# Kernel optimization log

Hardware: AMD Instinct MI355X
Metric: run time of the kernel (lower is better)

The kernel has to match this reference:

```python
import jax
import jax.numpy as jnp
import numpy as np
from jax import lax

B, L, A, C = 32, 128, 64, 128  # batch, length, n_agents, channels (in == out)
KT = 3                          # temporal kernel size, padding (KT-1)//2 keeps length


def setup_inputs() -> dict:
    key = jax.random.key(0)
    k1, k2, k3 = jax.random.split(key, 3)
    x = jax.random.normal(k1, (B, L, A, C), dtype=jnp.float32)
    # Conv2d weight [out_ch, in_ch, kt, 1] and bias, kaiming-ish scale
    W = jax.random.normal(k2, (C, C, KT, 1), dtype=jnp.float32) * (1.0 / np.sqrt(C * KT))
    b = jax.random.normal(k3, (C,), dtype=jnp.float32) * 0.01
    return {"x": x, "W": W, "b": b}


def reference(x, W, b):
    # x: [B, L, A, C] -> [B, C, L, A] (torch NCHW layout with H=time, W=agents)
    length, n_agents = x.shape[1], x.shape[2]
    xc = jnp.transpose(x, (0, 3, 1, 2))
    res = xc  # residual is identity (input_dim == output_dim, t_stride == 1)
    pad_t = (KT - 1) // 2
    y = lax.conv_general_dilated(
        xc, W,
        window_strides=(1, 1),
        padding=[(pad_t, pad_t), (0, 0)],
        dimension_numbers=("NCHW", "OIHW", "NCHW"),
    ) + b[None, :, None, None]  # [B, C, L, A]
    # Dense graph g[t,a,t',a'] = 1 iff t==t' or a==a'.  einsum('ncv,vw->ncw', x, g)
    # is exactly: sum over same time (all agents) + sum over same agent (all times) - self.
    agent_sum = jnp.sum(y, axis=3, keepdims=True)  # [B, C, L, 1]
    time_sum = jnp.sum(y, axis=2, keepdims=True)   # [B, C, 1, A]
    scale = (length + n_agents - 2) ** 0.5
    g = (agent_sum + time_sum - y) / scale
    out = jax.nn.relu(g + res)
    return jnp.transpose(out, (0, 2, 3, 1))  # [B, L, A, C]
```

## Files before the change

### kernel.cpp

```cpp
#include <hip/hip_runtime.h>
#include <stdint.h>


typedef __attribute__((ext_vector_type(8))) short bf16x8;
typedef __attribute__((ext_vector_type(4))) float f32x4;

__device__ __forceinline__ uint32_t f2bf(float f) {
    union { float f; uint32_t u; } v; v.f = f;
    return (v.u + 0x7FFFu + ((v.u >> 16) & 1u)) >> 16;
}
__device__ __forceinline__ float bf2f(uint32_t h) {
    union { uint32_t u; float f; } v; v.u = h << 16; return v.f;
}
__device__ __forceinline__ uint32_t pk2(float lo, float hi) {
    return f2bf(lo) | (f2bf(hi) << 16);
}

__global__ __launch_bounds__(256) void red_kernel(
    const float* __restrict__ x, uint16_t* __restrict__ xa16, float* __restrict__ xt_part,
    const float* __restrict__ W, uint16_t* __restrict__ wp)
{
    const int tid = threadIdx.x;
    const int bid = blockIdx.x;
    if (bid >= 512) {
        int o = (bid - 512) * 256 + tid;
        int i = o & 7, lane = (o >> 3) & 63, nt = (o >> 9) & 7, ks = (o >> 12) & 3, d = o >> 14;
        int ci = ks * 32 + (lane >> 4) * 8 + i;
        int co = nt * 16 + (lane & 15);
        wp[o] = (uint16_t)f2bf(W[(co * 128 + ci) * 3 + d]);
        return;
    }
    const int b = bid >> 4, g = bid & 15;
    const int ci8 = (tid & 15) * 8, ag = tid >> 4;
    __shared__ float red[16][128];

    float xtl[4][8];
    #pragma unroll
    for (int r = 0; r < 4; ++r)
        #pragma unroll
        for (int j = 0; j < 8; ++j) xtl[r][j] = 0.f;

    #pragma unroll
    for (int ti = 0; ti < 8; ++ti) {
        const int t = g * 8 + ti;
        const float* xr = x + ((size_t)(b * 128 + t) * 64) * 128;
        float s[8];
        #pragma unroll
        for (int j = 0; j < 8; ++j) s[j] = 0.f;
        #pragma unroll
        for (int r = 0; r < 4; ++r) {
            const int a = ag * 4 + r;
            const float4 v0 = *(const float4*)(xr + a * 128 + ci8);
            const float4 v1 = *(const float4*)(xr + a * 128 + ci8 + 4);
            s[0] += v0.x; s[1] += v0.y; s[2] += v0.z; s[3] += v0.w;
            s[4] += v1.x; s[5] += v1.y; s[6] += v1.z; s[7] += v1.w;
            xtl[r][0] += v0.x; xtl[r][1] += v0.y; xtl[r][2] += v0.z; xtl[r][3] += v0.w;
            xtl[r][4] += v1.x; xtl[r][5] += v1.y; xtl[r][6] += v1.z; xtl[r][7] += v1.w;
        }
        *(float4*)&red[ag][ci8]     = make_float4(s[0], s[1], s[2], s[3]);
        *(float4*)&red[ag][ci8 + 4] = make_float4(s[4], s[5], s[6], s[7]);
        __syncthreads();
        if (tid < 128) {
            float v = 0.f;
            #pragma unroll
            for (int i = 0; i < 16; ++i) v += red[i][tid];
            xa16[(size_t)(b * 130 + t + 1) * 128 + tid] = (uint16_t)f2bf(v);
        }
        __syncthreads();
    }
    if (g == 0 && tid < 16)
        *(uint4*)(xa16 + (size_t)(b * 130) * 128 + tid * 8) = make_uint4(0, 0, 0, 0);
    if (g == 15 && tid < 16)
        *(uint4*)(xa16 + (size_t)(b * 130 + 129) * 128 + tid * 8) = make_uint4(0, 0, 0, 0);
    #pragma unroll
    for (int r = 0; r < 4; ++r) {
        float* p = xt_part + (((size_t)(b * 16 + g) * 64 + ag * 4 + r) * 128) + ci8;
        *(float4*)p       = make_float4(xtl[r][0], xtl[r][1], xtl[r][2], xtl[r][3]);
        *(float4*)(p + 4) = make_float4(xtl[r][4], xtl[r][5], xtl[r][6], xtl[r][7]);
    }
}

__global__ __launch_bounds__(256) void xtr_kernel(
    const float* __restrict__ xt_part, float* __restrict__ xt)
{
    const int idx = blockIdx.x * 256 + threadIdx.x;
    const int row = idx >> 4, ci8 = (idx & 15) * 8;
    const int b = row >> 6, a = row & 63;
    float s[8];
    #pragma unroll
    for (int j = 0; j < 8; ++j) s[j] = 0.f;
    #pragma unroll
    for (int g2 = 0; g2 < 16; ++g2) {
        const float* p = xt_part + (((size_t)(b * 16 + g2) * 64 + a) * 128) + ci8;
        const float4 v0 = *(const float4*)p;
        const float4 v1 = *(const float4*)(p + 4);
        s[0] += v0.x; s[1] += v0.y; s[2] += v0.z; s[3] += v0.w;
        s[4] += v1.x; s[5] += v1.y; s[6] += v1.z; s[7] += v1.w;
    }
    float* q = xt + (size_t)row * 128 + ci8;
    *(float4*)q       = make_float4(s[0], s[1], s[2], s[3]);
    *(float4*)(q + 4) = make_float4(s[4], s[5], s[6], s[7]);
}

__global__ __launch_bounds__(256, 2) void sums_kernel(
    const uint16_t* __restrict__ xa16, const float* __restrict__ xt,
    const float* __restrict__ x, const uint16_t* __restrict__ wp,
    const float* __restrict__ bias, float* __restrict__ asum, float* __restrict__ tsum)
{
    __shared__ __align__(16) uint16_t slab[130 * 128];
    const int tid = threadIdx.x;
    const int lane = tid & 63, wid = tid >> 6;
    const int wm = wid >> 1, wn = wid & 1;
    const int lr = lane & 15, lg = lane >> 4;
    f32x4 acc[4][4];
    #pragma unroll
    for (int mi = 0; mi < 4; ++mi)
        #pragma unroll
        for (int ni = 0; ni < 4; ++ni) acc[mi][ni] = (f32x4)0.f;

    if (blockIdx.x < 32) {
        const int b = blockIdx.x;
        #pragma unroll
        for (int it = 0; it < 9; ++it) {
            const int gg = it * 256 + tid;
            if (gg < 2080) {
                const int row = gg >> 4, sp = gg & 15;
                const int sl = sp ^ (row & 7);
                *(uint4*)(slab + gg * 8) =
                    *(const uint4*)(xa16 + (size_t)(b * 130 + row) * 128 + sl * 8);
            }
        }
        __syncthreads();
        #pragma unroll
        for (int g = 0; g < 4; ++g)
            #pragma unroll
            for (int d = 0; d < 3; ++d) {
                bf16x8 bq[4], af[4];
                #pragma unroll
                for (int ni = 0; ni < 4; ++ni)
                    bq[ni] = *(const bf16x8*)(wp + (size_t)((((d * 4 + g) * 8) + wn * 4 + ni) * 64 + lane) * 8);
                #pragma unroll
                for (int mi = 0; mi < 4; ++mi) {
                    const int row = wm * 64 + mi * 16 + lr + d;
                    af[mi] = *(const bf16x8*)(slab + row * 128 + ((g * 4 + lg) ^ (row & 7)) * 8);
                }
                #pragma unroll
                for (int mi = 0; mi < 4; ++mi)
                    #pragma unroll
                    for (int ni = 0; ni < 4; ++ni)
                        acc[mi][ni] = __builtin_amdgcn_mfma_f32_16x16x32_bf16(af[mi], bq[ni], acc[mi][ni], 0, 0, 0);
            }
        #pragma unroll
        for (int ni = 0; ni < 4; ++ni) {
            const int col = wn * 64 + ni * 16 + lr;
            const float bv = 64.f * bias[col];
            #pragma unroll
            for (int mi = 0; mi < 4; ++mi)
                #pragma unroll
                for (int j = 0; j < 4; ++j) {
                    const int t = wm * 64 + mi * 16 + lg * 4 + j;
                    asum[((size_t)b * 128 + t) * 128 + col] = acc[mi][ni][j] + bv;
                }
        }
        return;
    }

    const int bid = blockIdx.x - 32;
    const int r = tid >> 1, h = tid & 1;
    const int grow = bid * 128 + r, sb = grow >> 6, sa = grow & 63;
    #pragma unroll
    for (int d = 0; d < 3; ++d) {
        {
            const float* Sp = xt + (size_t)grow * 128 + h * 64;
            const float* Ep = x + ((size_t)((sb * 128 + (d == 0 ? 127 : 0)) * 64 + sa)) * 128 + h * 64;
            #pragma unroll
            for (int k = 0; k < 8; ++k) {
                float4 f0 = *(const float4*)(Sp + k * 8);
                float4 f1 = *(const float4*)(Sp + k * 8 + 4);
                if (d != 1) {
                    const float4 e0 = *(const float4*)(Ep + k * 8);
                    const float4 e1 = *(const float4*)(Ep + k * 8 + 4);
                    f0.x -= e0.x; f0.y -= e0.y; f0.z -= e0.z; f0.w -= e0.w;
                    f1.x -= e1.x; f1.y -= e1.y; f1.z -= e1.z; f1.w -= e1.w;
                }
                uint4 o;
                o.x = pk2(f0.x, f0.y); o.y = pk2(f0.z, f0.w);
                o.z = pk2(f1.x, f1.y); o.w = pk2(f1.z, f1.w);
                const int sl = h * 8 + k;
                *(uint4*)(slab + r * 128 + (sl ^ (r & 7)) * 8) = o;
            }
        }
        __syncthreads();
        #pragma unroll
        for (int g = 0; g < 4; ++g) {
            bf16x8 bq[4], af[4];
            #pragma unroll
            for (int ni = 0; ni < 4; ++ni)
                bq[ni] = *(const bf16x8*)(wp + (size_t)((((d * 4 + g) * 8) + wn * 4 + ni) * 64 + lane) * 8);
            #pragma unroll
            for (int mi = 0; mi < 4; ++mi) {
                const int row = wm * 64 + mi * 16 + lr;
                af[mi] = *(const bf16x8*)(slab + row * 128 + ((g * 4 + lg) ^ (row & 7)) * 8);
            }
            #pragma unroll
            for (int mi = 0; mi < 4; ++mi)
                #pragma unroll
                for (int ni = 0; ni < 4; ++ni)
                    acc[mi][ni] = __builtin_amdgcn_mfma_f32_16x16x32_bf16(af[mi], bq[ni], acc[mi][ni], 0, 0, 0);
        }
        __syncthreads();
    }
    #pragma unroll
    for (int ni = 0; ni < 4; ++ni) {
        const int col = wn * 64 + ni * 16 + lr;
        const float bv = 128.f * bias[col];
        #pragma unroll
        for (int mi = 0; mi < 4; ++mi)
            #pragma unroll
            for (int j = 0; j < 4; ++j) {
                const int rg = bid * 128 + wm * 64 + mi * 16 + lg * 4 + j;
                tsum[(size_t)rg * 128 + col] = acc[mi][ni][j] + bv;
            }
    }
}

__global__ __launch_bounds__(512, 6) void conv_kernel(
    const float* __restrict__ x, const uint16_t* __restrict__ wp,
    const float* __restrict__ bias, const float* __restrict__ asum,
    const float* __restrict__ tsum, float* __restrict__ out)
{
    __shared__ __align__(16) uint16_t slab[2][192 * 64];
    const int tid = threadIdx.x;
    const int raw = blockIdx.x;
    const int bid = (raw & 7) * 512 + (raw >> 3);
    const int b = bid >> 7, t = bid & 127;
    const int lane = tid & 63, wid = tid >> 6;
    const int lr = lane & 15, lg = lane >> 4;

    f32x4 acc[4];
    #pragma unroll
    for (int mi = 0; mi < 4; ++mi) acc[mi] = (f32x4)0.f;

#define STAGE(c) do {                                                          \
    _Pragma("unroll")                                                          \
    for (int k = 0; k < 3; ++k) {                                              \
        const int ro  = lane >> 3;                                             \
        const int row = wid * 24 + k * 8 + ro;                                 \
        const int gl  = (lane & 7) ^ ro;                                       \
        const int tloc = t + (row >> 6) - 1;                                   \
        uint4 o4 = make_uint4(0, 0, 0, 0);                                     \
        if ((unsigned)tloc < 128u) {                                           \
            const float* s_ = x +                                              \
                ((size_t)((b * 128 + tloc) * 64 + (row & 63))) * 128 +         \
                (c) * 64 + gl * 8;                                             \
            const float4 v0 = *(const float4*)s_;                              \
            const float4 v1 = *(const float4*)(s_ + 4);                        \
            o4.x = pk2(v0.x, v0.y); o4.y = pk2(v0.z, v0.w);                    \
            o4.z = pk2(v1.x, v1.y); o4.w = pk2(v1.z, v1.w);                    \
        }                                                                      \
        *(uint4*)(&slab[c][wid * 1536 + k * 512 + lane * 8]) = o4;             \
    } } while (0)

#define MFMA_CHUNK(c) do {                                                     \
    _Pragma("unroll")                                                          \
    for (int d = 0; d < 3; ++d)                                                \
        _Pragma("unroll")                                                      \
        for (int g2 = 0; g2 < 2; ++g2) {                                       \
            const int ks = (c) * 2 + g2;                                       \
            bf16x8 bq, af[4];                                                  \
            bq = *(const bf16x8*)(wp +                                         \
                (size_t)((((d * 4 + ks) * 8) + wid) * 64 + lane) * 8);         \
            _Pragma("unroll")                                                  \
            for (int mi = 0; mi < 4; ++mi) {                                   \
                const int row = d * 64 + mi * 16 + lr;                         \
                af[mi] = *(const bf16x8*)(&slab[c][row * 64 +                  \
                    (((g2 * 4 + lg) ^ (row & 7)) * 8)]);                       \
            }                                                                  \
            _Pragma("unroll")                                                  \
            for (int mi = 0; mi < 4; ++mi)                                     \
                acc[mi] = __builtin_amdgcn_mfma_f32_16x16x32_bf16(             \
                    af[mi], bq, acc[mi], 0, 0, 0);                             \
        } } while (0)

    STAGE(0);
    __syncthreads();
    STAGE(1);
    MFMA_CHUNK(0);
    __syncthreads();
    MFMA_CHUNK(1);
    __syncthreads();

#undef STAGE
#undef MFMA_CHUNK

    {
        const int col = wid * 16 + lr;
        const float bv = bias[col];
        const int cbuf = col >> 6, cl = col & 63;
        #pragma unroll
        for (int mi = 0; mi < 4; ++mi)
            #pragma unroll
            for (int j = 0; j < 4; ++j) {
                const int a = mi * 16 + lg * 4 + j;
                slab[cbuf][a * 64 + (cl ^ ((a & 7) << 3))] = (uint16_t)f2bf(acc[mi][j] + bv);
            }
    }
    __syncthreads();

    {
        const float inv = 0.07254762501100116f;
        const int cg = tid & 15, rb = tid >> 4;
        const int cbuf = cg >> 3, cl8 = (cg & 7) * 8;
        const float* ap = asum + ((size_t)(b * 128 + t)) * 128 + cg * 8;
        const float4 as0 = *(const float4*)ap, as1 = *(const float4*)(ap + 4);
        const float av[8] = {as0.x, as0.y, as0.z, as0.w, as1.x, as1.y, as1.z, as1.w};
        #pragma unroll
        for (int j = 0; j < 2; ++j) {
            const int a = j * 32 + rb;
            const int swz = cl8 ^ ((a & 7) << 3);
            const uint4 yv = *(const uint4*)(&slab[cbuf][a * 64 + swz]);
            const uint4 xv = *(const uint4*)(&slab[cbuf][(64 + a) * 64 + swz]);
            const float* tp = tsum + ((size_t)(b * 64 + a)) * 128 + cg * 8;
            const float4 ts0 = *(const float4*)tp, ts1 = *(const float4*)(tp + 4);
            float yy[8], xx[8];
            yy[0] = bf2f(yv.x & 0xFFFFu); yy[1] = bf2f(yv.x >> 16);
            yy[2] = bf2f(yv.y & 0xFFFFu); yy[3] = bf2f(yv.y >> 16);
            yy[4] = bf2f(yv.z & 0xFFFFu); yy[5] = bf2f(yv.z >> 16);
            yy[6] = bf2f(yv.w & 0xFFFFu); yy[7] = bf2f(yv.w >> 16);
            xx[0] = bf2f(xv.x & 0xFFFFu); xx[1] = bf2f(xv.x >> 16);
            xx[2] = bf2f(xv.y & 0xFFFFu); xx[3] = bf2f(xv.y >> 16);
            xx[4] = bf2f(xv.z & 0xFFFFu); xx[5] = bf2f(xv.z >> 16);
            xx[6] = bf2f(xv.w & 0xFFFFu); xx[7] = bf2f(xv.w >> 16);
            const float tv[8] = {ts0.x, ts0.y, ts0.z, ts0.w, ts1.x, ts1.y, ts1.z, ts1.w};
            float o[8];
            #pragma unroll
            for (int i = 0; i < 8; ++i) {
                const float gg = (av[i] + tv[i] - yy[i]) * inv + xx[i];
                o[i] = gg > 0.f ? gg : 0.f;
            }
            float* op = out + ((size_t)((b * 128 + t) * 64 + a)) * 128 + cg * 8;
            *(float4*)op       = make_float4(o[0], o[1], o[2], o[3]);
            *(float4*)(op + 4) = make_float4(o[4], o[5], o[6], o[7]);
        }
    }
}

extern "C" void kernel_launch(void* const* d_in, const int* in_sizes, int n_in,
                              void* d_out, int out_size, void* d_ws, size_t ws_size,
                              hipStream_t stream) {
    const float* x    = (const float*)d_in[0];
    const float* W    = (const float*)d_in[1];
    const float* bias = (const float*)d_in[2];
    float* out = (float*)d_out;

    char* ws = (char*)d_ws;
    uint16_t* wp    = (uint16_t*)(ws);
    uint16_t* xa16  = (uint16_t*)(ws + 98304);
    float* xt_part  = (float*)(ws + 98304 + 1064960);
    float* xt       = (float*)(ws + 98304 + 1064960 + 16777216);
    float* asum     = (float*)(ws + 98304 + 1064960 + 16777216 + 1048576);
    float* tsum     = (float*)(ws + 98304 + 1064960 + 16777216 + 1048576 + 2097152);

    red_kernel  <<<704,  256, 0, stream>>>(x, xa16, xt_part, W, wp);
    xtr_kernel  <<<128,  256, 0, stream>>>(xt_part, xt);
    sums_kernel <<<48,   256, 0, stream>>>(xa16, xt, x, wp, bias, asum, tsum);
    conv_kernel <<<4096, 512, 0, stream>>>(x, wp, bias, asum, tsum, out);
}
```

Baseline: 114.9 us.

## Process eight timesteps per conv block with a rolling LDS ring of input slices

The conv kernel now handles 8 consecutive time steps per block instead of one, keeping a 4-slot LDS ring of bf16 input slices. Each x slice is loaded once and reused across the three temporal taps, where before each block re-read three slices. The next slice is prefetched into registers while MFMAs run on the current ones, and the tsum values are loaded once per block. The grid drops from 4096 to 512 blocks, which lowers parallelism and adds two barriers per step.

```diff
diff --git a/kernel.cpp b/kernel.cpp
--- a/kernel.cpp
+++ b/kernel.cpp
@@ -224,125 +224,143 @@
     }
 }
 
-__global__ __launch_bounds__(512, 6) void conv_kernel(
+__global__ __launch_bounds__(512, 4) void conv_kernel(
     const float* __restrict__ x, const uint16_t* __restrict__ wp,
     const float* __restrict__ bias, const float* __restrict__ asum,
     const float* __restrict__ tsum, float* __restrict__ out)
 {
-    __shared__ __align__(16) uint16_t slab[2][192 * 64];
+    __shared__ __align__(16) uint16_t ring[4][8192];
+    __shared__ __align__(16) uint16_t yb[8192];
+
     const int tid = threadIdx.x;
-    const int raw = blockIdx.x;
-    const int bid = (raw & 7) * 512 + (raw >> 3);
-    const int b = bid >> 7, t = bid & 127;
+    const int bid = blockIdx.x;
+    const int b = bid >> 4, t0 = (bid & 15) * 8;
     const int lane = tid & 63, wid = tid >> 6;
     const int lr = lane & 15, lg = lane >> 4;
 
-    f32x4 acc[4];
-    #pragma unroll
-    for (int mi = 0; mi < 4; ++mi) acc[mi] = (f32x4)0.f;
-
-#define STAGE(c) do {                                                          \
-    _Pragma("unroll")                                                          \
-    for (int k = 0; k < 3; ++k) {                                              \
-        const int ro  = lane >> 3;                                             \
-        const int row = wid * 24 + k * 8 + ro;                                 \
-        const int gl  = (lane & 7) ^ ro;                                       \
-        const int tloc = t + (row >> 6) - 1;                                   \
-        uint4 o4 = make_uint4(0, 0, 0, 0);                                     \
-        if ((unsigned)tloc < 128u) {                                           \
-            const float* s_ = x +                                              \
-                ((size_t)((b * 128 + tloc) * 64 + (row & 63))) * 128 +         \
-                (c) * 64 + gl * 8;                                             \
-            const float4 v0 = *(const float4*)s_;                              \
-            const float4 v1 = *(const float4*)(s_ + 4);                        \
-            o4.x = pk2(v0.x, v0.y); o4.y = pk2(v0.z, v0.w);                    \
-            o4.z = pk2(v1.x, v1.y); o4.w = pk2(v1.z, v1.w);                    \
-        }                                                                      \
-        *(uint4*)(&slab[c][wid * 1536 + k * 512 + lane * 8]) = o4;             \
+    const int srow = tid >> 3, pair = tid & 7, r7 = srow & 7;
+    const int sgbase = ((2 * pair) ^ r7) & ~1;
+    const bool sswap = (r7 & 1);
+    const float* xsrc0 = x + ((size_t)(b * 128) * 64 + srow) * 128 + sgbase * 8;
+    const int sdst = tid * 16;
+
+#define STAGE_LOAD(tau, h) do {                                                \
+    if ((unsigned)(tau) < 128u) {                                              \
+        const float* s_ = xsrc0 + (size_t)(tau) * 8192;                        \
+        h[0] = *(const float4*)s_;       h[1] = *(const float4*)(s_ + 4);      \
+        h[2] = *(const float4*)(s_ + 8); h[3] = *(const float4*)(s_ + 12);     \
+    } else {                                                                   \
+        h[0] = h[1] = h[2] = h[3] = make_float4(0.f, 0.f, 0.f, 0.f);           \
     } } while (0)
 
-#define MFMA_CHUNK(c) do {                                                     \
-    _Pragma("unroll")                                                          \
-    for (int d = 0; d < 3; ++d)                                                \
-        _Pragma("unroll")                                                      \
-        for (int g2 = 0; g2 < 2; ++g2) {                                       \
-            const int ks = (c) * 2 + g2;                                       \
-            bf16x8 bq, af[4];                                                  \
-            bq = *(const bf16x8*)(wp +                                         \
-                (size_t)((((d * 4 + ks) * 8) + wid) * 64 + lane) * 8);         \
-            _Pragma("unroll")                                                  \
-            for (int mi = 0; mi < 4; ++mi) {                                   \
-                const int row = d * 64 + mi * 16 + lr;                         \
-                af[mi] = *(const bf16x8*)(&slab[c][row * 64 +                  \
-                    (((g2 * 4 + lg) ^ (row & 7)) * 8)]);                       \
-            }                                                                  \
-            _Pragma("unroll")                                                  \
-            for (int mi = 0; mi < 4; ++mi)                                     \
-                acc[mi] = __builtin_amdgcn_mfma_f32_16x16x32_bf16(             \
-                    af[mi], bq, acc[mi], 0, 0, 0);                             \
-        } } while (0)
-
-    STAGE(0);
+#define STAGE_WRITE(slot, h) do {                                              \
+    uint4 lo_, hi_;                                                            \
+    lo_.x = pk2(h[0].x, h[0].y); lo_.y = pk2(h[0].z, h[0].w);                  \
+    lo_.z = pk2(h[1].x, h[1].y); lo_.w = pk2(h[1].z, h[1].w);                  \
+    hi_.x = pk2(h[2].x, h[2].y); hi_.y = pk2(h[2].z, h[2].w);                  \
+    hi_.z = pk2(h[3].x, h[3].y); hi_.w = pk2(h[3].z, h[3].w);                  \
+    *(uint4*)(&ring[slot][sdst])     = sswap ? hi_ : lo_;                      \
+    *(uint4*)(&ring[slot][sdst + 8]) = sswap ? lo_ : hi_;                      \
+    } while (0)
+
+    {
+        float4 h[4];
+        STAGE_LOAD(t0 - 1, h); STAGE_WRITE(0, h);
+        STAGE_LOAD(t0,     h); STAGE_WRITE(1, h);
+        STAGE_LOAD(t0 + 1, h); STAGE_WRITE(2, h);
+    }
     __syncthreads();
-    STAGE(1);
-    MFMA_CHUNK(0);
-    __syncthreads();
-    MFMA_CHUNK(1);
-    __syncthreads();
-
-#undef STAGE
-#undef MFMA_CHUNK
-
-    {
-        const int col = wid * 16 + lr;
-        const float bv = bias[col];
-        const int cbuf = col >> 6, cl = col & 63;
+
+    const int col = wid * 16 + lr;
+    const float bvc = bias[col];
+    const int cg = tid & 15, rb = tid >> 4;
+    float tv[2][8];
+    #pragma unroll
+    for (int j = 0; j < 2; ++j) {
+        const int a = j * 32 + rb;
+        const float* tp = tsum + ((size_t)(b * 64 + a)) * 128 + cg * 8;
+        const float4 t0v = *(const float4*)tp, t1v = *(const float4*)(tp + 4);
+        tv[j][0] = t0v.x; tv[j][1] = t0v.y; tv[j][2] = t0v.z; tv[j][3] = t0v.w;
+        tv[j][4] = t1v.x; tv[j][5] = t1v.y; tv[j][6] = t1v.z; tv[j][7] = t1v.w;
+    }
+
+    #pragma unroll
+    for (int ti = 0; ti < 8; ++ti) {
+        const int t = t0 + ti;
+        float4 h[4];
+        if (ti < 7) STAGE_LOAD(t + 2, h);
+
+        f32x4 acc[4];
+        #pragma unroll
+        for (int mi = 0; mi < 4; ++mi) acc[mi] = (f32x4)0.f;
+
+        #pragma unroll
+        for (int d = 0; d < 3; ++d) {
+            const int slot = (ti + d) & 3;
+            #pragma unroll
+            for (int g = 0; g < 4; ++g) {
+                bf16x8 bq, af[4];
+                bq = *(const bf16x8*)(wp + (size_t)((((d * 4 + g) * 8) + wid) * 64 + lane) * 8);
+                #pragma unroll
+                for (int mi = 0; mi < 4; ++mi) {
+                    const int row = mi * 16 + lr;
+                    af[mi] = *(const bf16x8*)(&ring[slot][row * 128 + (((g * 4 + lg) ^ (row & 7)) * 8)]);
+                }
+                #pragma unroll
+                for (int mi = 0; mi < 4; ++mi)
+                    acc[mi] = __builtin_amdgcn_mfma_f32_16x16x32_bf16(af[mi], bq, acc[mi], 0, 0, 0);
+            }
+        }
+
         #pragma unroll
         for (int mi = 0; mi < 4; ++mi)
             #pragma unroll
             for (int j = 0; j < 4; ++j) {
                 const int a = mi * 16 + lg * 4 + j;
-                slab[cbuf][a * 64 + (cl ^ ((a & 7) << 3))] = (uint16_t)f2bf(acc[mi][j] + bv);
-            }
-    }
-    __syncthreads();
-
-    {
-        const float inv = 0.07254762501100116f;
-        const int cg = tid & 15, rb = tid >> 4;
-        const int cbuf = cg >> 3, cl8 = (cg & 7) * 8;
-        const float* ap = asum + ((size_t)(b * 128 + t)) * 128 + cg * 8;
-        const float4 as0 = *(const float4*)ap, as1 = *(const float4*)(ap + 4);
-        const float av[8] = {as0.x, as0.y, as0.z, as0.w, as1.x, as1.y, as1.z, as1.w};
-        #pragma unroll
-        for (int j = 0; j < 2; ++j) {
-            const int a = j * 32 + rb;
-            const int swz = cl8 ^ ((a & 7) << 3);
-            const uint4 yv = *(const uint4*)(&slab[cbuf][a * 64 + swz]);
-            const uint4 xv = *(const uint4*)(&slab[cbuf][(64 + a) * 64 + swz]);
-            const float* tp = tsum + ((size_t)(b * 64 + a)) * 128 + cg * 8;
-            const float4 ts0 = *(const float4*)tp, ts1 = *(const float4*)(tp + 4);
-            float yy[8], xx[8];
-            yy[0] = bf2f(yv.x & 0xFFFFu); yy[1] = bf2f(yv.x >> 16);
-            yy[2] = bf2f(yv.y & 0xFFFFu); yy[3] = bf2f(yv.y >> 16);
-            yy[4] = bf2f(yv.z & 0xFFFFu); yy[5] = bf2f(yv.z >> 16);
-            yy[6] = bf2f(yv.w & 0xFFFFu); yy[7] = bf2f(yv.w >> 16);
-            xx[0] = bf2f(xv.x & 0xFFFFu); xx[1] = bf2f(xv.x >> 16);
-            xx[2] = bf2f(xv.y & 0xFFFFu); xx[3] = bf2f(xv.y >> 16);
-            xx[4] = bf2f(xv.z & 0xFFFFu); xx[5] = bf2f(xv.z >> 16);
-            xx[6] = bf2f(xv.w & 0xFFFFu); xx[7] = bf2f(xv.w >> 16);
-            const float tv[8] = {ts0.x, ts0.y, ts0.z, ts0.w, ts1.x, ts1.y, ts1.z, ts1.w};
-            float o[8];
-            #pragma unroll
-            for (int i = 0; i < 8; ++i) {
-                const float gg = (av[i] + tv[i] - yy[i]) * inv + xx[i];
-                o[i] = gg > 0.f ? gg : 0.f;
-            }
-            float* op = out + ((size_t)((b * 128 + t) * 64 + a)) * 128 + cg * 8;
-            *(float4*)op       = make_float4(o[0], o[1], o[2], o[3]);
-            *(float4*)(op + 4) = make_float4(o[4], o[5], o[6], o[7]);
-        }
-    }
+                yb[a * 128 + (col ^ ((a & 7) << 3))] = (uint16_t)f2bf(acc[mi][j] + bvc);
+            }
+
+        if (ti < 7) STAGE_WRITE((ti + 3) & 3, h);
+
+        __syncthreads();
+
+        {
+            const float inv = 0.07254762501100116f;
+            const float* ap = asum + ((size_t)(b * 128 + t)) * 128 + cg * 8;
+            const float4 as0 = *(const float4*)ap, as1 = *(const float4*)(ap + 4);
+            const float av[8] = {as0.x, as0.y, as0.z, as0.w, as1.x, as1.y, as1.z, as1.w};
+            const int cslot = (ti + 1) & 3;
+            #pragma unroll
+            for (int j = 0; j < 2; ++j) {
+                const int a = j * 32 + rb;
+                const int el = (cg ^ (a & 7)) * 8;
+                const uint4 yv = *(const uint4*)(&yb[a * 128 + el]);
+                const uint4 xv = *(const uint4*)(&ring[cslot][a * 128 + el]);
+                float yy[8], xx[8];
+                yy[0] = bf2f(yv.x & 0xFFFFu); yy[1] = bf2f(yv.x >> 16);
+                yy[2] = bf2f(yv.y & 0xFFFFu); yy[3] = bf2f(yv.y >> 16);
+                yy[4] = bf2f(yv.z & 0xFFFFu); yy[5] = bf2f(yv.z >> 16);
+                yy[6] = bf2f(yv.w & 0xFFFFu); yy[7] = bf2f(yv.w >> 16);
+                xx[0] = bf2f(xv.x & 0xFFFFu); xx[1] = bf2f(xv.x >> 16);
+                xx[2] = bf2f(xv.y & 0xFFFFu); xx[3] = bf2f(xv.y >> 16);
+                xx[4] = bf2f(xv.z & 0xFFFFu); xx[5] = bf2f(xv.z >> 16);
+                xx[6] = bf2f(xv.w & 0xFFFFu); xx[7] = bf2f(xv.w >> 16);
+                float o[8];
+                #pragma unroll
+                for (int i = 0; i < 8; ++i) {
+                    const float gg = (av[i] + tv[j][i] - yy[i]) * inv + xx[i];
+                    o[i] = gg > 0.f ? gg : 0.f;
+                }
+                float* op = out + ((size_t)((b * 128 + t) * 64 + a)) * 128 + cg * 8;
+                *(float4*)op       = make_float4(o[0], o[1], o[2], o[3]);
+                *(float4*)(op + 4) = make_float4(o[4], o[5], o[6], o[7]);
+            }
+        }
+        __syncthreads();
+    }
+
+#undef STAGE_LOAD
+#undef STAGE_WRITE
 }
 
 extern "C" void kernel_launch(void* const* d_in, const int* in_sizes, int n_in,
@@ -361,8 +379,8 @@
     float* asum     = (float*)(ws + 98304 + 1064960 + 16777216 + 1048576);
     float* tsum     = (float*)(ws + 98304 + 1064960 + 16777216 + 1048576 + 2097152);
 
-    red_kernel  <<<704,  256, 0, stream>>>(x, xa16, xt_part, W, wp);
-    xtr_kernel  <<<128,  256, 0, stream>>>(xt_part, xt);
-    sums_kernel <<<48,   256, 0, stream>>>(xa16, xt, x, wp, bias, asum, tsum);
-    conv_kernel <<<4096, 512, 0, stream>>>(x, wp, bias, asum, tsum, out);
-}
+    red_kernel  <<<704, 256, 0, stream>>>(x, xa16, xt_part, W, wp);
+    xtr_kernel  <<<128, 256, 0, stream>>>(xt_part, xt);
+    sums_kernel <<<48,  256, 0, stream>>>(xa16, xt, x, wp, bias, asum, tsum);
+    conv_kernel <<<512, 512, 0, stream>>>(x, wp, bias, asum, tsum, out);
+}
```

Measured after the change: 128.8 us. 1.12x slower.
